# Performance work log

Measured on AMD Instinct MI355X. Metric: run time of the kernel, lower is better.

Reference implementation:

```python
import jax, jax.numpy as jnp
import numpy as np
from jax import lax

B, S, IN, D, E, NH = 8, 128, 512, 1024, 4, 16
DH = D // NH
EPS = 1e-5
SCALE = np.float32(1.0 / np.sqrt(DH))


def setup_inputs() -> dict:
    key = jax.random.key(0)
    ks = iter(jax.random.split(key, 64))
    def rn(shape, scale=0.02):
        return jax.random.normal(next(ks), shape, dtype=jnp.float32) * scale
    z = lambda shape: jnp.zeros(shape, dtype=jnp.float32)
    return {
        "x": jax.random.normal(next(ks), (B, S, IN), dtype=jnp.float32),
        "router_w": rn((IN, E)), "router_b": z((E,)),
        "enc_w1": rn((E, IN, D)), "enc_b1": z((E, D)),
        "enc_w2": rn((E, D, D)), "enc_b2": z((E, D)),
        "enc_g": jnp.ones((E, D), jnp.float32), "enc_beta": z((E, D)),
        "attn_in_w": rn((E, D, 3 * D)), "attn_in_b": z((E, 3 * D)),
        "attn_out_w": rn((E, D, D)), "attn_out_b": z((E, D)),
        "lstm_wi_f": rn((E, D, 4 * D)), "lstm_wh_f": rn((E, D, 4 * D)), "lstm_b_f": z((E, 4 * D)),
        "lstm_wi_b": rn((E, D, 4 * D)), "lstm_wh_b": rn((E, D, 4 * D)), "lstm_b_b": z((E, 4 * D)),
        "sig_w1": rn((E, 2 * D, D)), "sig_b1": z((E, D)),
        "sig_w2": rn((E, D, D)), "sig_b2": z((E, D)),
        "tan_w1": rn((E, 2 * D, D)), "tan_b1": z((E, D)),
        "tan_w2": rn((E, D, D)), "tan_b2": z((E, D)),
        "dec_w1": rn((E, D, D)), "dec_b1": z((E, D)),
        "dec_w2": rn((E, D, IN)), "dec_b2": z((E, IN)),
        "dec_g": jnp.ones((E, IN), jnp.float32), "dec_beta": z((E, IN)),
    }


def _ln(x, g, b):
    m = x.mean(-1, keepdims=True)
    v = ((x - m) ** 2).mean(-1, keepdims=True)
    return (x - m) * lax.rsqrt(v + EPS) * g + b


def _lstm_dir(x, Wi, Wh, b):
    # x: [B,S,D]; single-direction LSTM, returns h sequence [B,S,H]
    bsz = x.shape[0]
    h0 = jnp.zeros((bsz, Wh.shape[0]), x.dtype)
    def step(carry, xt):
        h, c = carry
        zg = xt @ Wi + h @ Wh + b  # [B,4H]; torch gate order i,f,g,o
        i, f, g, o = jnp.split(zg, 4, axis=-1)
        c = jax.nn.sigmoid(f) * c + jax.nn.sigmoid(i) * jnp.tanh(g)
        h = jax.nn.sigmoid(o) * jnp.tanh(c)
        return (h, c), h
    _, hs = lax.scan(step, (h0, h0), jnp.swapaxes(x, 0, 1))
    return jnp.swapaxes(hs, 0, 1)


def _expert(x, p):
    (ew1, eb1, ew2, eb2, eg, ebeta, aiw, aib, aow, aob,
     wif, whf, bf, wibk, whbk, bbk, sw1, sb1, sw2, sb2,
     tw1, tb1, tw2, tb2, dw1, db1, dw2, db2, dg, dbeta) = p
    # encoder MLP + LayerNorm
    h = _ln(jax.nn.relu(x @ ew1 + eb1) @ ew2 + eb2, eg, ebeta)  # [B,S,D]
    # full self-attention (torch MultiheadAttention)
    qkv = h @ aiw + aib
    q, k, v = jnp.split(qkv, 3, axis=-1)
    def heads(t):
        return t.reshape(t.shape[0], t.shape[1], NH, DH).transpose(0, 2, 1, 3)
    q, k, v = heads(q), heads(k), heads(v)
    attn = jax.nn.softmax(jnp.einsum('bhqd,bhkd->bhqk', q, k) * SCALE, axis=-1)
    o = jnp.einsum('bhqk,bhkd->bhqd', attn, v).transpose(0, 2, 1, 3).reshape(h.shape)
    h = o @ aow + aob
    # bidirectional LSTM memory
    hf = _lstm_dir(h, wif, whf, bf)
    hb = _lstm_dir(h[:, ::-1], wibk, whbk, bbk)[:, ::-1]
    mem = jnp.concatenate([hf, hb], axis=-1)  # [B,S,2D]
    # sigmoid/tanh gate branches multiplied
    gate_s = jax.nn.sigmoid(jax.nn.relu(mem @ sw1 + sb1) @ sw2 + sb2)
    gate_t = jnp.tanh(jax.nn.relu(mem @ tw1 + tb1) @ tw2 + tb2)
    g = gate_s * gate_t  # [B,S,D]
    # decoder MLP + LayerNorm back to input_dim
    return _ln(jax.nn.relu(g @ dw1 + db1) @ dw2 + db2, dg, dbeta)


def _forward(x, router_w, router_b, *p):
    outs = jax.vmap(lambda pe: _expert(x, pe))(tuple(p))  # [E,B,S,IN]
    w = jax.nn.softmax(x @ router_w + router_b, axis=-1)  # [B,S,E] token-level routing
    return jnp.einsum('ebsd,bse->bsd', outs, w)


def reference(x, router_w, router_b, enc_w1, enc_b1, enc_w2, enc_b2, enc_g, enc_beta,
              attn_in_w, attn_in_b, attn_out_w, attn_out_b,
              lstm_wi_f, lstm_wh_f, lstm_b_f, lstm_wi_b, lstm_wh_b, lstm_b_b,
              sig_w1, sig_b1, sig_w2, sig_b2, tan_w1, tan_b1, tan_w2, tan_b2,
              dec_w1, dec_b1, dec_w2, dec_b2, dec_g, dec_beta):
    return _forward(x, router_w, router_b, enc_w1, enc_b1, enc_w2, enc_b2, enc_g, enc_beta,
                    attn_in_w, attn_in_b, attn_out_w, attn_out_b,
                    lstm_wi_f, lstm_wh_f, lstm_b_f, lstm_wi_b, lstm_wh_b, lstm_b_b,
                    sig_w1, sig_b1, sig_w2, sig_b2, tan_w1, tan_b1, tan_w2, tan_b2,
                    dec_w1, dec_b1, dec_w2, dec_b2, dec_g, dec_beta)
```

## Files before the change

kernel.cpp:

```cpp
#include <hip/hip_runtime.h>


typedef __attribute__((ext_vector_type(8))) short short8v;
typedef __attribute__((ext_vector_type(4))) float float4v;

__device__ __forceinline__ float bf2f(unsigned short u) {
    unsigned int x = ((unsigned int)u) << 16;
    return __builtin_bit_cast(float, x);
}
__device__ __forceinline__ unsigned short f2bf(float f) {
    unsigned int u = __builtin_bit_cast(unsigned int, f);
    u += 0x7fffu + ((u >> 16) & 1u);
    return (unsigned short)(u >> 16);
}
__device__ __forceinline__ void gload_lds16(const unsigned short* g, unsigned short* lds) {
    __builtin_amdgcn_global_load_lds(
        (const __attribute__((address_space(1))) unsigned int*)g,
        (__attribute__((address_space(3))) unsigned int*)lds, 16, 0, 0);
}

__global__ __launch_bounds__(256) void cvt_bf16_kernel(
    const float* __restrict__ in, unsigned short* __restrict__ out, int n4)
{
    int i = blockIdx.x * 256 + threadIdx.x;
    if (i >= n4) return;
    float4 v = *reinterpret_cast<const float4*>(&in[i * 4]);
    ushort4 o;
    o.x = f2bf(v.x); o.y = f2bf(v.y); o.z = f2bf(v.z); o.w = f2bf(v.w);
    *reinterpret_cast<ushort4*>(&out[i * 4]) = o;
}

struct TransJobs {
    const float* src[14];
    unsigned short* dst[14];
    int K[14], N[14];
    int prefix[15];
    long sWe[14], sTe[14];
};

__global__ __launch_bounds__(256) void transpose_all(TransJobs J)
{
    __shared__ float tile[32][33];
    int bid = blockIdx.x;
    int j = 0;
    #pragma unroll
    for (int i = 0; i < 14; ++i) if (bid >= J.prefix[i + 1]) j = i + 1;
    int lb = bid - J.prefix[j];
    int K = J.K[j], N = J.N[j];
    int tn = N >> 5, tk = K >> 5;
    int e = lb / (tn * tk), rem = lb % (tn * tk);
    int ky = rem / tn, nx = rem % tn;
    const float* W = J.src[j] + (long)e * J.sWe[j];
    unsigned short* Wt = J.dst[j] + (long)e * J.sTe[j];
    int k0 = ky * 32, n0 = nx * 32;
    int tx = threadIdx.x & 31, ty = threadIdx.x >> 5;
    #pragma unroll
    for (int i = 0; i < 32; i += 8)
        tile[ty + i][tx] = W[(long)(k0 + ty + i) * N + n0 + tx];
    __syncthreads();
    #pragma unroll
    for (int i = 0; i < 32; i += 8)
        Wt[(long)(n0 + ty + i) * K + k0 + tx] = f2bf(tile[tx][ty + i]);
}

__global__ __launch_bounds__(64) void router_kernel(
    const float* __restrict__ x, const float* __restrict__ rw,
    const float* __restrict__ rb, float* __restrict__ router)
{
    int token = blockIdx.x;
    int lane = threadIdx.x;
    float a0 = 0.f, a1 = 0.f, a2 = 0.f, a3 = 0.f;
    const float* xp = x + (long)token * 512;
    for (int i = lane; i < 512; i += 64) {
        float xv = xp[i];
        const float* w = rw + (long)i * 4;
        a0 += xv * w[0]; a1 += xv * w[1]; a2 += xv * w[2]; a3 += xv * w[3];
    }
    #pragma unroll
    for (int off = 32; off; off >>= 1) {
        a0 += __shfl_down(a0, off); a1 += __shfl_down(a1, off);
        a2 += __shfl_down(a2, off); a3 += __shfl_down(a3, off);
    }
    if (lane == 0) {
        a0 += rb[0]; a1 += rb[1]; a2 += rb[2]; a3 += rb[3];
        float m = fmaxf(fmaxf(a0, a1), fmaxf(a2, a3));
        float e0 = __expf(a0 - m), e1 = __expf(a1 - m);
        float e2 = __expf(a2 - m), e3 = __expf(a3 - m);
        float inv = 1.f / (e0 + e1 + e2 + e3);
        *reinterpret_cast<float4*>(&router[token * 4]) =
            make_float4(e0 * inv, e1 * inv, e2 * inv, e3 * inv);
    }
}

template <int OUTBF>
__global__ __launch_bounds__(256) void gemm_bf16(
    const unsigned short* __restrict__ A, const unsigned short* __restrict__ Wt,
    const float* __restrict__ bias, const float* __restrict__ bias2,
    const unsigned short* __restrict__ mul,
    void* __restrict__ Cv, int N, int K, int lda, int nsplit,
    long sAe, long sWe, long sBe, long sMe, long sCe, int act)
{
    __shared__ unsigned short As[2][128 * 64];
    __shared__ unsigned short Bs[2][128 * 64];
    int e = blockIdx.z;
    A += (long)e * sAe; Wt += (long)e * sWe;
    bias += (long)e * sBe; bias2 += (long)e * sBe;
    if (mul) mul += (long)e * sMe;
    int tid = threadIdx.x;
    int row0 = blockIdx.y * 128, col0 = blockIdx.x * 128;
    int wid = tid >> 6, lane = tid & 63;
    int wr = wid >> 1, wc = wid & 1;
    int l15 = lane & 15, l4 = lane >> 4;
    int r8 = lane >> 3, sg = lane & 7;
    float4v acc[4][4];
    #pragma unroll
    for (int i = 0; i < 4; ++i)
        #pragma unroll
        for (int j = 0; j < 4; ++j) acc[i][j] = (float4v){0.f, 0.f, 0.f, 0.f};

    auto STAGE = [&](int buf, int k0) {
        #pragma unroll
        for (int c = 0; c < 4; ++c) {
            int chunk = wid * 4 + c;
            int rowA = chunk * 8 + r8;
            int segA = (sg ^ (rowA & 7)) * 8;
            gload_lds16(A + (long)(row0 + rowA) * lda + k0 + segA,
                        (unsigned short*)((char*)As[buf] + chunk * 1024));
            gload_lds16(Wt + (long)(col0 + rowA) * K + k0 + segA,
                        (unsigned short*)((char*)Bs[buf] + chunk * 1024));
        }
    };
    int nt = K >> 6;
    STAGE(0, 0);
    for (int t = 0; t < nt; ++t) {
        int cur = t & 1;
        if (t + 1 < nt) {
            STAGE(cur ^ 1, (t + 1) << 6);
            asm volatile("s_waitcnt vmcnt(8)" ::: "memory");
        } else {
            asm volatile("s_waitcnt vmcnt(0)" ::: "memory");
        }
        __builtin_amdgcn_s_barrier();
        __builtin_amdgcn_sched_barrier(0);
        #pragma unroll
        for (int kk = 0; kk < 2; ++kk) {
            short8v af[4], bq[4];
            int bytec = kk * 64 + l4 * 16;
            #pragma unroll
            for (int m = 0; m < 4; ++m) {
                int r = wr * 64 + m * 16 + l15;
                af[m] = *reinterpret_cast<const short8v*>(
                    (char*)As[cur] + r * 128 + (bytec ^ ((r & 7) << 4)));
            }
            #pragma unroll
            for (int n = 0; n < 4; ++n) {
                int r = wc * 64 + n * 16 + l15;
                bq[n] = *reinterpret_cast<const short8v*>(
                    (char*)Bs[cur] + r * 128 + (bytec ^ ((r & 7) << 4)));
            }
            #pragma unroll
            for (int m = 0; m < 4; ++m)
                #pragma unroll
                for (int n = 0; n < 4; ++n)
                    acc[m][n] = __builtin_amdgcn_mfma_f32_16x16x32_bf16(
                        af[m], bq[n], acc[m][n], 0, 0, 0);
        }
        __builtin_amdgcn_sched_barrier(0);
        __builtin_amdgcn_s_barrier();
    }
    float* Cf = (float*)Cv + (long)e * sCe;
    unsigned short* Cb = (unsigned short*)Cv + (long)e * sCe;
    #pragma unroll
    for (int n = 0; n < 4; ++n) {
        int col = col0 + wc * 64 + n * 16 + l15;
        float bia = (col < nsplit) ? bias[col] : bias2[col - nsplit];
        #pragma unroll
        for (int m = 0; m < 4; ++m) {
            #pragma unroll
            for (int r = 0; r < 4; ++r) {
                long row = row0 + wr * 64 + m * 16 + l4 * 4 + r;
                float v = acc[m][n][r] + bia;
                if (act == 1) v = fmaxf(v, 0.f);
                else if (act == 2) v = 1.f / (1.f + __expf(-v));
                else if (act == 3) v = tanhf(v);
                if (mul) v *= bf2f(mul[row * N + col]);
                if (OUTBF) Cb[row * N + col] = f2bf(v);
                else       Cf[row * N + col] = v;
            }
        }
    }
}

template <int DIM>
__global__ __launch_bounds__(256) void ln_bf16(
    unsigned short* __restrict__ buf, const float* __restrict__ g,
    const float* __restrict__ beta)
{
    constexpr int PT = DIM / 256;
    __shared__ float sbuf[4];
    int row = blockIdx.x, e = row >> 10;
    unsigned short* p = buf + (long)row * DIM;
    const float* gp = g + (long)e * DIM;
    const float* bp = beta + (long)e * DIM;
    int tid = threadIdx.x;
    float v[PT];
    ushort4 u = *reinterpret_cast<const ushort4*>(p + tid * PT);
    v[0] = bf2f(u.x); v[1] = bf2f(u.y); v[2] = bf2f(u.z); v[3] = bf2f(u.w);
    float s = v[0] + v[1] + v[2] + v[3];
    #pragma unroll
    for (int off = 32; off; off >>= 1) s += __shfl_down(s, off);
    if ((tid & 63) == 0) sbuf[tid >> 6] = s;
    __syncthreads();
    float mean = (sbuf[0] + sbuf[1] + sbuf[2] + sbuf[3]) / (float)DIM;
    __syncthreads();
    float vs = 0.f;
    #pragma unroll
    for (int i = 0; i < PT; ++i) { float d = v[i] - mean; vs += d * d; }
    #pragma unroll
    for (int off = 32; off; off >>= 1) vs += __shfl_down(vs, off);
    if ((tid & 63) == 0) sbuf[tid >> 6] = vs;
    __syncthreads();
    float var = (sbuf[0] + sbuf[1] + sbuf[2] + sbuf[3]) / (float)DIM;
    float rstd = rsqrtf(var + 1e-5f);
    ushort4 o;
    o.x = f2bf((v[0] - mean) * rstd * gp[tid * PT + 0] + bp[tid * PT + 0]);
    o.y = f2bf((v[1] - mean) * rstd * gp[tid * PT + 1] + bp[tid * PT + 1]);
    o.z = f2bf((v[2] - mean) * rstd * gp[tid * PT + 2] + bp[tid * PT + 2]);
    o.w = f2bf((v[3] - mean) * rstd * gp[tid * PT + 3] + bp[tid * PT + 3]);
    *reinterpret_cast<ushort4*>(p + tid * PT) = o;
}

template <int DIM>
__global__ __launch_bounds__(256) void ln_kernel(
    float* __restrict__ buf, const float* __restrict__ g,
    const float* __restrict__ beta)
{
    constexpr int PT = DIM / 256;
    __shared__ float sbuf[4];
    int row = blockIdx.x, e = row >> 10;
    float* p = buf + (long)row * DIM;
    const float* gp = g + (long)e * DIM;
    const float* bp = beta + (long)e * DIM;
    int tid = threadIdx.x;
    float v[PT];
    float s = 0.f;
    #pragma unroll
    for (int i = 0; i < PT; ++i) { v[i] = p[tid + i * 256]; s += v[i]; }
    #pragma unroll
    for (int off = 32; off; off >>= 1) s += __shfl_down(s, off);
    if ((tid & 63) == 0) sbuf[tid >> 6] = s;
    __syncthreads();
    float mean = (sbuf[0] + sbuf[1] + sbuf[2] + sbuf[3]) / (float)DIM;
    __syncthreads();
    float vs = 0.f;
    #pragma unroll
    for (int i = 0; i < PT; ++i) { float d = v[i] - mean; vs += d * d; }
    #pragma unroll
    for (int off = 32; off; off >>= 1) vs += __shfl_down(vs, off);
    if ((tid & 63) == 0) sbuf[tid >> 6] = vs;
    __syncthreads();
    float var = (sbuf[0] + sbuf[1] + sbuf[2] + sbuf[3]) / (float)DIM;
    float rstd = rsqrtf(var + 1e-5f);
    #pragma unroll
    for (int i = 0; i < PT; ++i)
        p[tid + i * 256] = (v[i] - mean) * rstd * gp[tid + i * 256] + bp[tid + i * 256];
}

__global__ __launch_bounds__(128) void attn_bf16(
    const unsigned short* __restrict__ qkv, unsigned short* __restrict__ o)
{
    __shared__ __align__(16) float Ks[128][64];
    __shared__ __align__(16) float Vs[128][64];
    int id = blockIdx.x;
    int hd = id & 15, b = (id >> 4) & 7, e = id >> 7;
    int tid = threadIdx.x;
    const long base = ((long)e * 1024 + b * 128) * 3072 + hd * 64;
    #pragma unroll
    for (int i = 0; i < 8; ++i) {
        int idx = i * 128 + tid;
        int row = idx >> 3, f8 = (idx & 7) * 8;
        short8v kv = *reinterpret_cast<const short8v*>(&qkv[base + (long)row * 3072 + 1024 + f8]);
        short8v vv = *reinterpret_cast<const short8v*>(&qkv[base + (long)row * 3072 + 2048 + f8]);
        #pragma unroll
        for (int j = 0; j < 8; ++j) {
            Ks[row][f8 + j] = bf2f((unsigned short)kv[j]);
            Vs[row][f8 + j] = bf2f((unsigned short)vv[j]);
        }
    }
    __syncthreads();
    float q[64];
    #pragma unroll
    for (int f = 0; f < 8; ++f) {
        short8v qv = *reinterpret_cast<const short8v*>(&qkv[base + (long)tid * 3072 + f * 8]);
        #pragma unroll
        for (int j = 0; j < 8; ++j) q[f * 8 + j] = bf2f((unsigned short)qv[j]);
    }
    float m = -__builtin_huge_valf(), l = 0.f;
    float oa[64];
    #pragma unroll
    for (int d = 0; d < 64; ++d) oa[d] = 0.f;
    for (int j = 0; j < 128; ++j) {
        float s = 0.f;
        #pragma unroll
        for (int d = 0; d < 64; ++d) s = fmaf(q[d], Ks[j][d], s);
        s *= 0.125f;
        float mn = fmaxf(m, s);
        float corr = __expf(m - mn);
        float pj = __expf(s - mn);
        l = l * corr + pj;
        #pragma unroll
        for (int d = 0; d < 64; ++d) oa[d] = oa[d] * corr + pj * Vs[j][d];
        m = mn;
    }
    float inv = 1.f / l;
    unsigned short* op = o + ((long)e * 1024 + b * 128 + tid) * 1024 + hd * 64;
    #pragma unroll
    for (int f = 0; f < 8; ++f) {
        short8v ov;
        #pragma unroll
        for (int j = 0; j < 8; ++j) ov[j] = (short)f2bf(oa[f * 8 + j] * inv);
        *reinterpret_cast<short8v*>(&op[f * 8]) = ov;
    }
}

__global__ __launch_bounds__(512, 4) void lstm_persistent(
    const unsigned short* __restrict__ pre, const unsigned short* __restrict__ whtf,
    const unsigned short* __restrict__ whtb, unsigned short* __restrict__ hstate,
    unsigned short* __restrict__ memb, unsigned int* __restrict__ sync)
{
    __shared__ unsigned short hA[16 * 1024];
    __shared__ float zred[4][2][8][16];
    int bid = blockIdx.x;
    int ed = bid & 7, cb = bid >> 3;
    int e = ed >> 1, dir = ed & 1;
    const unsigned short* Wt = (dir ? whtb : whtf) + (long)e * 4096 * 1024;
    unsigned int* arr = sync + ed * 64;
    int tid = threadIdx.x;
    int w = tid >> 6, lane = tid & 63, l15 = lane & 15, l4 = lane >> 4;
    int g = w >> 1, kh = w & 1;
    short8v wf[16];
    const unsigned short* wp =
        Wt + ((long)(g * 1024 + cb * 16 + l15)) * 1024 + kh * 512 + l4 * 8;
    #pragma unroll
    for (int ks = 0; ks < 16; ++ks)
        wf[ks] = *reinterpret_cast<const short8v*>(wp + ks * 32);
    short8v z8 = {0, 0, 0, 0, 0, 0, 0, 0};
    for (int i = tid; i < 8 * 128; i += 512) {
        int r = 8 + (i >> 7), sb = (i & 127) * 16;
        *reinterpret_cast<short8v*>((char*)hA + r * 2048 + (sb ^ ((r & 7) << 4))) = z8;
    }
    float c0 = 0.f, c1 = 0.f;
    int gp = tid & 7, gb = tid >> 3;
    for (int s = 0; s < 128; ++s) {
        int t = dir ? 127 - s : s;
        const unsigned long long* hin64 = reinterpret_cast<const unsigned long long*>(
            hstate + (long)(s & 1) * 65536 + (long)ed * 8192);
        __syncthreads();
        #pragma unroll
        for (int i = 0; i < 4; ++i) {
            int idx = tid + 512 * i;
            unsigned long long v = __hip_atomic_load(
                hin64 + idx, __ATOMIC_RELAXED, __HIP_MEMORY_SCOPE_AGENT);
            int r = idx >> 8, sb = (idx & 255) * 8;
            *reinterpret_cast<unsigned long long*>(
                (char*)hA + r * 2048 + (sb ^ ((r & 7) << 4))) = v;
        }
        float pz[8];
        if (tid < 64) {
            const unsigned short* prow =
                pre + (((long)e * 1024) + gb * 128 + t) * 8192 + dir * 4096 + cb * 16 + gp * 2;
            #pragma unroll
            for (int gg = 0; gg < 4; ++gg) {
                unsigned int u = *reinterpret_cast<const unsigned int*>(prow + gg * 1024);
                pz[gg * 2]     = bf2f((unsigned short)(u & 0xffff));
                pz[gg * 2 + 1] = bf2f((unsigned short)(u >> 16));
            }
        }
        __syncthreads();
        float4v acc = (float4v){0.f, 0.f, 0.f, 0.f};
        int abase = l15 * 2048, aswz = (l15 & 7) << 4;
        #pragma unroll
        for (int ks = 0; ks < 16; ++ks) {
            short8v a = *reinterpret_cast<const short8v*>(
                (char*)hA + abase + (((kh * 512 + ks * 32) * 2 + l4 * 16) ^ aswz));
            acc = __builtin_amdgcn_mfma_f32_16x16x32_bf16(a, wf[ks], acc, 0, 0, 0);
        }
        if (l4 < 2) {
            #pragma unroll
            for (int r = 0; r < 4; ++r)
                zred[g][kh][l4 * 4 + r][l15] = acc[r];
        }
        __syncthreads();
        if (tid < 64) {
            int col0 = gp * 2;
            float h2[2];
            #pragma unroll
            for (int cc = 0; cc < 2; ++cc) {
                int col = col0 + cc;
                float zi = zred[0][0][gb][col] + zred[0][1][gb][col] + pz[0 + cc];
                float zf = zred[1][0][gb][col] + zred[1][1][gb][col] + pz[2 + cc];
                float zg = zred[2][0][gb][col] + zred[2][1][gb][col] + pz[4 + cc];
                float zo = zred[3][0][gb][col] + zred[3][1][gb][col] + pz[6 + cc];
                float ig = 1.f / (1.f + __expf(-zi));
                float fg = 1.f / (1.f + __expf(-zf));
                float gv = tanhf(zg);
                float og = 1.f / (1.f + __expf(-zo));
                float cv = cc ? c1 : c0;
                cv = fg * cv + ig * gv;
                if (cc) c1 = cv; else c0 = cv;
                h2[cc] = og * tanhf(cv);
            }
            unsigned int hv = (unsigned int)f2bf(h2[0]) | ((unsigned int)f2bf(h2[1]) << 16);
            int hcol = cb * 16 + col0;
            unsigned int* hout32 = reinterpret_cast<unsigned int*>(
                hstate + (long)((s & 1) ^ 1) * 65536 + (long)ed * 8192);
            __hip_atomic_store(hout32 + (gb * 1024 + hcol) / 2, hv,
                               __ATOMIC_RELAXED, __HIP_MEMORY_SCOPE_AGENT);
            *reinterpret_cast<unsigned int*>(
                memb + (((long)e * 8 + gb) * 128 + t) * 2048 + dir * 1024 + hcol) = hv;
        }
        if (s == 127) break;
        __syncthreads();
        if (tid == 0)
            __hip_atomic_store(arr + cb, (unsigned)(s + 1), __ATOMIC_RELAXED,
                               __HIP_MEMORY_SCOPE_AGENT);
        if (tid < 64) {
            while (__hip_atomic_load(arr + tid, __ATOMIC_RELAXED,
                                     __HIP_MEMORY_SCOPE_AGENT) < (unsigned)(s + 1))
                __builtin_amdgcn_s_sleep(1);
        }
    }
}

__global__ __launch_bounds__(256) void combine_kernel(
    const float* __restrict__ outs, const float* __restrict__ router,
    float* __restrict__ out)
{
    int idx = blockIdx.x * 256 + threadIdx.x;
    int token = idx >> 7, q = (idx & 127) * 4;
    float4 r = *reinterpret_cast<const float4*>(&router[token * 4]);
    const float* bp = outs + (long)token * 512 + q;
    float4 v0 = *reinterpret_cast<const float4*>(bp);
    float4 v1 = *reinterpret_cast<const float4*>(bp + 524288);
    float4 v2 = *reinterpret_cast<const float4*>(bp + 1048576);
    float4 v3 = *reinterpret_cast<const float4*>(bp + 1572864);
    float4 a;
    a.x = r.x * v0.x + r.y * v1.x + r.z * v2.x + r.w * v3.x;
    a.y = r.x * v0.y + r.y * v1.y + r.z * v2.y + r.w * v3.y;
    a.z = r.x * v0.z + r.y * v1.z + r.z * v2.z + r.w * v3.z;
    a.w = r.x * v0.w + r.y * v1.w + r.z * v2.w + r.w * v3.w;
    *reinterpret_cast<float4*>(&out[(long)token * 512 + q]) = a;
}

extern "C" void kernel_launch(void* const* d_in, const int* in_sizes, int n_in,
                              void* d_out, int out_size, void* d_ws, size_t ws_size,
                              hipStream_t stream)
{
    (void)in_sizes; (void)n_in; (void)out_size; (void)ws_size;
    const float* x        = (const float*)d_in[0];
    const float* router_w = (const float*)d_in[1];
    const float* router_b = (const float*)d_in[2];
    const float* enc_w1   = (const float*)d_in[3];
    const float* enc_b1   = (const float*)d_in[4];
    const float* enc_w2   = (const float*)d_in[5];
    const float* enc_b2   = (const float*)d_in[6];
    const float* enc_g    = (const float*)d_in[7];
    const float* enc_beta = (const float*)d_in[8];
    const float* aiw      = (const float*)d_in[9];
    const float* aib      = (const float*)d_in[10];
    const float* aow      = (const float*)d_in[11];
    const float* aob      = (const float*)d_in[12];
    const float* wif      = (const float*)d_in[13];
    const float* whf      = (const float*)d_in[14];
    const float* bfv      = (const float*)d_in[15];
    const float* wib      = (const float*)d_in[16];
    const float* whb      = (const float*)d_in[17];
    const float* bbv      = (const float*)d_in[18];
    const float* sw1      = (const float*)d_in[19];
    const float* sb1      = (const float*)d_in[20];
    const float* sw2      = (const float*)d_in[21];
    const float* sb2      = (const float*)d_in[22];
    const float* tw1      = (const float*)d_in[23];
    const float* tb1      = (const float*)d_in[24];
    const float* tw2      = (const float*)d_in[25];
    const float* tb2      = (const float*)d_in[26];
    const float* dw1      = (const float*)d_in[27];
    const float* db1      = (const float*)d_in[28];
    const float* dw2      = (const float*)d_in[29];
    const float* db2      = (const float*)d_in[30];
    const float* dg       = (const float*)d_in[31];
    const float* dbeta    = (const float*)d_in[32];
    float* out = (float*)d_out;

    const long m = 1024L * 1024L;
    unsigned short* U = (unsigned short*)d_ws;
    unsigned short* ew1T = U;
    unsigned short* ew2T = U + 2 * m;
    unsigned short* aiwT = U + 6 * m;
    unsigned short* aowT = U + 18 * m;
    unsigned short* wiT  = U + 22 * m;
    unsigned short* whtf = U + 54 * m;
    unsigned short* whtb = U + 70 * m;
    unsigned short* gw1T = U + 86 * m;
    unsigned short* sw2T = U + 102 * m;
    unsigned short* tw2T = U + 106 * m;
    unsigned short* dw1T = U + 110 * m;
    unsigned short* dw2T = U + 114 * m;
    unsigned short* xb   = U + 116 * m;
    unsigned short* hbuf = xb + 524288;
    unsigned short* t1   = hbuf + 4 * m;
    unsigned short* t2   = t1 + 4 * m;
    unsigned short* pre  = t2 + 4 * m;
    unsigned short* memb = pre + 32 * m;
    unsigned short* hstate = memb + 8 * m;
    float* F      = (float*)(U + 170 * m);
    float* outs   = F;
    float* router = outs + 2 * m;
    unsigned int* syncv = (unsigned int*)(router + 4096);

    hipMemsetAsync(hstate, 0, 65536 * sizeof(unsigned short), stream);
    hipMemsetAsync(syncv, 0, 1024 * sizeof(unsigned int), stream);

    cvt_bf16_kernel<<<512, 256, 0, stream>>>(x, xb, 131072);
    {
        TransJobs J;
        const float* srcs[14] = {enc_w1, enc_w2, aiw, aow, wif, wib, whf, whb,
                                 sw1, tw1, sw2, tw2, dw1, dw2};
        unsigned short* dsts[14] = {ew1T, ew2T, aiwT, aowT, wiT, wiT + 4096 * 1024L,
                                    whtf, whtb, gw1T, gw1T + 2 * m, sw2T, tw2T, dw1T, dw2T};
        int Ks[14] = {512, 1024, 1024, 1024, 1024, 1024, 1024, 1024,
                      2048, 2048, 1024, 1024, 1024, 1024};
        int Ns[14] = {1024, 1024, 3072, 1024, 4096, 4096, 4096, 4096,
                      1024, 1024, 1024, 1024, 1024, 512};
        long sWes[14] = {512 * 1024L, m, 3 * m, m, 4 * m, 4 * m, 4 * m, 4 * m,
                         2 * m, 2 * m, m, m, m, 512 * 1024L};
        long sTes[14] = {512 * 1024L, m, 3 * m, m, 8 * m, 8 * m, 4 * m, 4 * m,
                         4 * m, 4 * m, m, m, m, 512 * 1024L};
        int pfx = 0;
        J.prefix[0] = 0;
        for (int i = 0; i < 14; ++i) {
            J.src[i] = srcs[i]; J.dst[i] = dsts[i];
            J.K[i] = Ks[i]; J.N[i] = Ns[i];
            J.sWe[i] = sWes[i]; J.sTe[i] = sTes[i];
            pfx += (Ns[i] >> 5) * (Ks[i] >> 5) * 4;
            J.prefix[i + 1] = pfx;
        }
        transpose_all<<<pfx, 256, 0, stream>>>(J);
    }

    router_kernel<<<1024, 64, 0, stream>>>(x, router_w, router_b, router);

    gemm_bf16<1><<<dim3(8, 8, 4), 256, 0, stream>>>(xb, ew1T, enc_b1, enc_b1, nullptr, t1,
        1024, 512, 512, 1024, 0L, 512 * 1024L, 1024L, 0L, m, 1);
    gemm_bf16<1><<<dim3(8, 8, 4), 256, 0, stream>>>(t1, ew2T, enc_b2, enc_b2, nullptr, hbuf,
        1024, 1024, 1024, 1024, m, m, 1024L, 0L, m, 0);
    ln_bf16<1024><<<4096, 256, 0, stream>>>(hbuf, enc_g, enc_beta);
    gemm_bf16<1><<<dim3(24, 8, 4), 256, 0, stream>>>(hbuf, aiwT, aib, aib, nullptr, pre,
        3072, 1024, 1024, 3072, m, 3 * m, 3072L, 0L, 3 * m, 0);
    attn_bf16<<<512, 128, 0, stream>>>(pre, t1);
    gemm_bf16<1><<<dim3(8, 8, 4), 256, 0, stream>>>(t1, aowT, aob, aob, nullptr, hbuf,
        1024, 1024, 1024, 1024, m, m, 1024L, 0L, m, 0);
    gemm_bf16<1><<<dim3(64, 8, 4), 256, 0, stream>>>(hbuf, wiT, bfv, bbv, nullptr, pre,
        8192, 1024, 1024, 4096, m, 8 * m, 4096L, 0L, 8 * m, 0);
    lstm_persistent<<<512, 512, 0, stream>>>(pre, whtf, whtb, hstate, memb, syncv);
    unsigned short* g1o = pre;
    gemm_bf16<1><<<dim3(16, 8, 4), 256, 0, stream>>>(memb, gw1T, sb1, tb1, nullptr, g1o,
        2048, 2048, 2048, 1024, 2 * m, 4 * m, 1024L, 0L, 2 * m, 1);
    gemm_bf16<1><<<dim3(8, 8, 4), 256, 0, stream>>>(g1o, sw2T, sb2, sb2, nullptr, t2,
        1024, 1024, 2048, 1024, 2 * m, m, 1024L, 0L, m, 2);
    gemm_bf16<1><<<dim3(8, 8, 4), 256, 0, stream>>>(g1o + 1024, tw2T, tb2, tb2, t2, hbuf,
        1024, 1024, 2048, 1024, 2 * m, m, 1024L, m, m, 3);
    gemm_bf16<1><<<dim3(8, 8, 4), 256, 0, stream>>>(hbuf, dw1T, db1, db1, nullptr, t1,
        1024, 1024, 1024, 1024, m, m, 1024L, 0L, m, 1);
    gemm_bf16<0><<<dim3(4, 8, 4), 256, 0, stream>>>(t1, dw2T, db2, db2, nullptr, outs,
        512, 1024, 1024, 512, m, 512 * 1024L, 512L, 0L, 512 * 1024L, 0);
    ln_kernel<512><<<4096, 256, 0, stream>>>(outs, dg, dbeta);
    combine_kernel<<<512, 256, 0, stream>>>(outs, router, out);
}
```

Baseline: 1.306 ms.

## Replace LSTM inter-block barrier with tagged-data flags embedded in hidden state

The persistent LSTM kernel no longer uses a separate per-step arrival counter and spin barrier. Each block now writes the hidden state as fp32, with the low mantissa bit carrying a parity tag that encodes the step. Consumers poll the state words directly until every tag matches, then convert to bf16 in LDS. This removes one __syncthreads, the counter store and the barrier round trip on the serial 128-step critical path, at the cost of twice the hidden-state traffic, more polling loads per thread, and a small precision change from overwriting the mantissa bit.

Result: slower. 1.769 ms (+35.4%).

```diff
diff --git a/kernel.cpp b/kernel.cpp
--- a/kernel.cpp
+++ b/kernel.cpp
@@ -325,8 +325,8 @@
 
 __global__ __launch_bounds__(512, 4) void lstm_persistent(
     const unsigned short* __restrict__ pre, const unsigned short* __restrict__ whtf,
-    const unsigned short* __restrict__ whtb, unsigned short* __restrict__ hstate,
-    unsigned short* __restrict__ memb, unsigned int* __restrict__ sync)
+    const unsigned short* __restrict__ whtb, float* __restrict__ hstate,
+    unsigned short* __restrict__ memb)
 {
     __shared__ unsigned short hA[16 * 1024];
     __shared__ float zred[4][2][8][16];
@@ -334,7 +334,6 @@
     int ed = bid & 7, cb = bid >> 3;
     int e = ed >> 1, dir = ed & 1;
     const unsigned short* Wt = (dir ? whtb : whtf) + (long)e * 4096 * 1024;
-    unsigned int* arr = sync + ed * 64;
     int tid = threadIdx.x;
     int w = tid >> 6, lane = tid & 63, l15 = lane & 15, l4 = lane >> 4;
     int g = w >> 1, kh = w & 1;
@@ -353,18 +352,10 @@
     int gp = tid & 7, gb = tid >> 3;
     for (int s = 0; s < 128; ++s) {
         int t = dir ? 127 - s : s;
+        unsigned tag_r = (s == 0) ? 0u : ((((unsigned)(s - 1)) >> 1) + 1u) & 1u;
         const unsigned long long* hin64 = reinterpret_cast<const unsigned long long*>(
             hstate + (long)(s & 1) * 65536 + (long)ed * 8192);
         __syncthreads();
-        #pragma unroll
-        for (int i = 0; i < 4; ++i) {
-            int idx = tid + 512 * i;
-            unsigned long long v = __hip_atomic_load(
-                hin64 + idx, __ATOMIC_RELAXED, __HIP_MEMORY_SCOPE_AGENT);
-            int r = idx >> 8, sb = (idx & 255) * 8;
-            *reinterpret_cast<unsigned long long*>(
-                (char*)hA + r * 2048 + (sb ^ ((r & 7) << 4))) = v;
-        }
         float pz[8];
         if (tid < 64) {
             const unsigned short* prow =
@@ -375,6 +366,40 @@
                 pz[gg * 2]     = bf2f((unsigned short)(u & 0xffff));
                 pz[gg * 2 + 1] = bf2f((unsigned short)(u >> 16));
             }
+        }
+        unsigned long long v[8];
+        #pragma unroll
+        for (int i = 0; i < 8; ++i)
+            v[i] = __hip_atomic_load(hin64 + tid + 512 * i,
+                                     __ATOMIC_RELAXED, __HIP_MEMORY_SCOPE_AGENT);
+        unsigned pend = 0xffu;
+        while (true) {
+            unsigned np = 0;
+            #pragma unroll
+            for (int i = 0; i < 8; ++i) {
+                if (pend & (1u << i)) {
+                    unsigned lo = (unsigned)v[i], hi = (unsigned)(v[i] >> 32);
+                    if ((((lo ^ tag_r) | (hi ^ tag_r)) & 1u)) np |= 1u << i;
+                }
+            }
+            if (!np) break;
+            __builtin_amdgcn_s_sleep(1);
+            #pragma unroll
+            for (int i = 0; i < 8; ++i)
+                if (np & (1u << i))
+                    v[i] = __hip_atomic_load(hin64 + tid + 512 * i,
+                                             __ATOMIC_RELAXED, __HIP_MEMORY_SCOPE_AGENT);
+            pend = np;
+        }
+        #pragma unroll
+        for (int i = 0; i < 8; ++i) {
+            int idx = tid + 512 * i;
+            float f0 = __builtin_bit_cast(float, (unsigned)v[i]);
+            float f1 = __builtin_bit_cast(float, (unsigned)(v[i] >> 32));
+            unsigned hv = (unsigned)f2bf(f0) | ((unsigned)f2bf(f1) << 16);
+            int r = idx >> 9, ob = (idx & 511) * 4;
+            *reinterpret_cast<unsigned*>(
+                (char*)hA + r * 2048 + (ob ^ ((r & 7) << 4))) = hv;
         }
         __syncthreads();
         float4v acc = (float4v){0.f, 0.f, 0.f, 0.f};
@@ -410,24 +435,19 @@
                 if (cc) c1 = cv; else c0 = cv;
                 h2[cc] = og * tanhf(cv);
             }
-            unsigned int hv = (unsigned int)f2bf(h2[0]) | ((unsigned int)f2bf(h2[1]) << 16);
             int hcol = cb * 16 + col0;
-            unsigned int* hout32 = reinterpret_cast<unsigned int*>(
+            unsigned hv = (unsigned)f2bf(h2[0]) | ((unsigned)f2bf(h2[1]) << 16);
+            *reinterpret_cast<unsigned*>(
+                memb + (((long)e * 8 + gb) * 128 + t) * 2048 + dir * 1024 + hcol) = hv;
+            unsigned tw = ((((unsigned)s) >> 1) + 1u) & 1u;
+            unsigned u0 = (__builtin_bit_cast(unsigned, h2[0]) & ~1u) | tw;
+            unsigned u1 = (__builtin_bit_cast(unsigned, h2[1]) & ~1u) | tw;
+            unsigned long long uv = (unsigned long long)u0 |
+                                    ((unsigned long long)u1 << 32);
+            unsigned long long* hout64 = reinterpret_cast<unsigned long long*>(
                 hstate + (long)((s & 1) ^ 1) * 65536 + (long)ed * 8192);
-            __hip_atomic_store(hout32 + (gb * 1024 + hcol) / 2, hv,
+            __hip_atomic_store(hout64 + (gb * 1024 + hcol) / 2, uv,
                                __ATOMIC_RELAXED, __HIP_MEMORY_SCOPE_AGENT);
-            *reinterpret_cast<unsigned int*>(
-                memb + (((long)e * 8 + gb) * 128 + t) * 2048 + dir * 1024 + hcol) = hv;
-        }
-        if (s == 127) break;
-        __syncthreads();
-        if (tid == 0)
-            __hip_atomic_store(arr + cb, (unsigned)(s + 1), __ATOMIC_RELAXED,
-                               __HIP_MEMORY_SCOPE_AGENT);
-        if (tid < 64) {
-            while (__hip_atomic_load(arr + tid, __ATOMIC_RELAXED,
-                                     __HIP_MEMORY_SCOPE_AGENT) < (unsigned)(s + 1))
-                __builtin_amdgcn_s_sleep(1);
         }
     }
 }
@@ -512,14 +532,12 @@
     unsigned short* t2   = t1 + 4 * m;
     unsigned short* pre  = t2 + 4 * m;
     unsigned short* memb = pre + 32 * m;
-    unsigned short* hstate = memb + 8 * m;
     float* F      = (float*)(U + 170 * m);
     float* outs   = F;
     float* router = outs + 2 * m;
-    unsigned int* syncv = (unsigned int*)(router + 4096);
-
-    hipMemsetAsync(hstate, 0, 65536 * sizeof(unsigned short), stream);
-    hipMemsetAsync(syncv, 0, 1024 * sizeof(unsigned int), stream);
+    float* hstateF = router + 4096;
+
+    hipMemsetAsync(hstateF, 0, 65536 * sizeof(float), stream);
 
     cvt_bf16_kernel<<<512, 256, 0, stream>>>(x, xb, 131072);
     {
@@ -562,7 +580,7 @@
         1024, 1024, 1024, 1024, m, m, 1024L, 0L, m, 0);
     gemm_bf16<1><<<dim3(64, 8, 4), 256, 0, stream>>>(hbuf, wiT, bfv, bbv, nullptr, pre,
         8192, 1024, 1024, 4096, m, 8 * m, 4096L, 0L, 8 * m, 0);
-    lstm_persistent<<<512, 512, 0, stream>>>(pre, whtf, whtb, hstate, memb, syncv);
+    lstm_persistent<<<512, 512, 0, stream>>>(pre, whtf, whtb, hstateF, memb);
     unsigned short* g1o = pre;
     gemm_bf16<1><<<dim3(16, 8, 4), 256, 0, stream>>>(memb, gw1T, sb1, tb1, nullptr, g1o,
         2048, 2048, 2048, 1024, 2 * m, 4 * m, 1024L, 0L, 2 * m, 1);
```

## Replace LSTM per-step counter barrier with sentinel-poisoned h sequence polling

Applied to the files above, without the earlier changes.

The persistent LSTM kernel no longer uses a per-step atomic counter barrier across blocks. Each step's hidden state goes to its own slot in a sequence buffer pre-filled with a 0x7f7f sentinel, and readers spin on the data itself until no sentinel values remain. This removes one barrier round-trip and the extra __syncthreads per timestep. It also swaps tanhf for an exp-based fast tanh. The risks are that a real bf16 value equal to 0x7f7f would cause a hang, and that the fast tanh loses some accuracy and can produce NaN for large inputs where exp overflows.

After: 1.419 ms. 1.09x slower.

```diff
diff --git a/kernel.cpp b/kernel.cpp
--- a/kernel.cpp
+++ b/kernel.cpp
@@ -17,6 +17,15 @@
     __builtin_amdgcn_global_load_lds(
         (const __attribute__((address_space(1))) unsigned int*)g,
         (__attribute__((address_space(3))) unsigned int*)lds, 16, 0, 0);
+}
+__device__ __forceinline__ float ftanh(float x) {
+    float e = __expf(2.f * x);
+    return 1.f - 2.f / (e + 1.f);
+}
+__device__ __forceinline__ bool stale8(unsigned long long x) {
+    unsigned lo = (unsigned)x, hi = (unsigned)(x >> 32);
+    return ((lo & 0xffffu) == 0x7f7fu) | ((lo >> 16) == 0x7f7fu) |
+           ((hi & 0xffffu) == 0x7f7fu) | ((hi >> 16) == 0x7f7fu);
 }
 
 __global__ __launch_bounds__(256) void cvt_bf16_kernel(
@@ -182,7 +191,7 @@
                 float v = acc[m][n][r] + bia;
                 if (act == 1) v = fmaxf(v, 0.f);
                 else if (act == 2) v = 1.f / (1.f + __expf(-v));
-                else if (act == 3) v = tanhf(v);
+                else if (act == 3) v = ftanh(v);
                 if (mul) v *= bf2f(mul[row * N + col]);
                 if (OUTBF) Cb[row * N + col] = f2bf(v);
                 else       Cf[row * N + col] = v;
@@ -325,8 +334,8 @@
 
 __global__ __launch_bounds__(512, 4) void lstm_persistent(
     const unsigned short* __restrict__ pre, const unsigned short* __restrict__ whtf,
-    const unsigned short* __restrict__ whtb, unsigned short* __restrict__ hstate,
-    unsigned short* __restrict__ memb, unsigned int* __restrict__ sync)
+    const unsigned short* __restrict__ whtb, unsigned short* __restrict__ hseq,
+    unsigned short* __restrict__ memb)
 {
     __shared__ unsigned short hA[16 * 1024];
     __shared__ float zred[4][2][8][16];
@@ -334,7 +343,6 @@
     int ed = bid & 7, cb = bid >> 3;
     int e = ed >> 1, dir = ed & 1;
     const unsigned short* Wt = (dir ? whtb : whtf) + (long)e * 4096 * 1024;
-    unsigned int* arr = sync + ed * 64;
     int tid = threadIdx.x;
     int w = tid >> 6, lane = tid & 63, l15 = lane & 15, l4 = lane >> 4;
     int g = w >> 1, kh = w & 1;
@@ -354,17 +362,8 @@
     for (int s = 0; s < 128; ++s) {
         int t = dir ? 127 - s : s;
         const unsigned long long* hin64 = reinterpret_cast<const unsigned long long*>(
-            hstate + (long)(s & 1) * 65536 + (long)ed * 8192);
+            hseq + ((long)s * 8 + ed) * 8192);
         __syncthreads();
-        #pragma unroll
-        for (int i = 0; i < 4; ++i) {
-            int idx = tid + 512 * i;
-            unsigned long long v = __hip_atomic_load(
-                hin64 + idx, __ATOMIC_RELAXED, __HIP_MEMORY_SCOPE_AGENT);
-            int r = idx >> 8, sb = (idx & 255) * 8;
-            *reinterpret_cast<unsigned long long*>(
-                (char*)hA + r * 2048 + (sb ^ ((r & 7) << 4))) = v;
-        }
         float pz[8];
         if (tid < 64) {
             const unsigned short* prow =
@@ -375,6 +374,34 @@
                 pz[gg * 2]     = bf2f((unsigned short)(u & 0xffff));
                 pz[gg * 2 + 1] = bf2f((unsigned short)(u >> 16));
             }
+        }
+        unsigned long long v[4];
+        #pragma unroll
+        for (int i = 0; i < 4; ++i)
+            v[i] = __hip_atomic_load(hin64 + tid + 512 * i,
+                                     __ATOMIC_RELAXED, __HIP_MEMORY_SCOPE_AGENT);
+        unsigned pend = 0xfu;
+        while (true) {
+            unsigned np = 0;
+            #pragma unroll
+            for (int i = 0; i < 4; ++i)
+                if ((pend >> i) & 1u)
+                    if (stale8(v[i])) np |= 1u << i;
+            if (!np) break;
+            __builtin_amdgcn_s_sleep(1);
+            #pragma unroll
+            for (int i = 0; i < 4; ++i)
+                if ((np >> i) & 1u)
+                    v[i] = __hip_atomic_load(hin64 + tid + 512 * i,
+                                             __ATOMIC_RELAXED, __HIP_MEMORY_SCOPE_AGENT);
+            pend = np;
+        }
+        #pragma unroll
+        for (int i = 0; i < 4; ++i) {
+            int idx = tid + 512 * i;
+            int r = idx >> 8, sb = (idx & 255) * 8;
+            *reinterpret_cast<unsigned long long*>(
+                (char*)hA + r * 2048 + (sb ^ ((r & 7) << 4))) = v[i];
         }
         __syncthreads();
         float4v acc = (float4v){0.f, 0.f, 0.f, 0.f};
@@ -403,31 +430,21 @@
                 float zo = zred[3][0][gb][col] + zred[3][1][gb][col] + pz[6 + cc];
                 float ig = 1.f / (1.f + __expf(-zi));
                 float fg = 1.f / (1.f + __expf(-zf));
-                float gv = tanhf(zg);
+                float gv = ftanh(zg);
                 float og = 1.f / (1.f + __expf(-zo));
                 float cv = cc ? c1 : c0;
                 cv = fg * cv + ig * gv;
                 if (cc) c1 = cv; else c0 = cv;
-                h2[cc] = og * tanhf(cv);
+                h2[cc] = og * ftanh(cv);
             }
             unsigned int hv = (unsigned int)f2bf(h2[0]) | ((unsigned int)f2bf(h2[1]) << 16);
             int hcol = cb * 16 + col0;
             unsigned int* hout32 = reinterpret_cast<unsigned int*>(
-                hstate + (long)((s & 1) ^ 1) * 65536 + (long)ed * 8192);
+                hseq + ((long)(s + 1) * 8 + ed) * 8192);
             __hip_atomic_store(hout32 + (gb * 1024 + hcol) / 2, hv,
                                __ATOMIC_RELAXED, __HIP_MEMORY_SCOPE_AGENT);
             *reinterpret_cast<unsigned int*>(
                 memb + (((long)e * 8 + gb) * 128 + t) * 2048 + dir * 1024 + hcol) = hv;
-        }
-        if (s == 127) break;
-        __syncthreads();
-        if (tid == 0)
-            __hip_atomic_store(arr + cb, (unsigned)(s + 1), __ATOMIC_RELAXED,
-                               __HIP_MEMORY_SCOPE_AGENT);
-        if (tid < 64) {
-            while (__hip_atomic_load(arr + tid, __ATOMIC_RELAXED,
-                                     __HIP_MEMORY_SCOPE_AGENT) < (unsigned)(s + 1))
-                __builtin_amdgcn_s_sleep(1);
         }
     }
 }
@@ -512,14 +529,10 @@
     unsigned short* t2   = t1 + 4 * m;
     unsigned short* pre  = t2 + 4 * m;
     unsigned short* memb = pre + 32 * m;
-    unsigned short* hstate = memb + 8 * m;
     float* F      = (float*)(U + 170 * m);
     float* outs   = F;
     float* router = outs + 2 * m;
-    unsigned int* syncv = (unsigned int*)(router + 4096);
-
-    hipMemsetAsync(hstate, 0, 65536 * sizeof(unsigned short), stream);
-    hipMemsetAsync(syncv, 0, 1024 * sizeof(unsigned int), stream);
+    unsigned short* hseq = U;
 
     cvt_bf16_kernel<<<512, 256, 0, stream>>>(x, xb, 131072);
     {
@@ -562,7 +575,10 @@
         1024, 1024, 1024, 1024, m, m, 1024L, 0L, m, 0);
     gemm_bf16<1><<<dim3(64, 8, 4), 256, 0, stream>>>(hbuf, wiT, bfv, bbv, nullptr, pre,
         8192, 1024, 1024, 4096, m, 8 * m, 4096L, 0L, 8 * m, 0);
-    lstm_persistent<<<512, 512, 0, stream>>>(pre, whtf, whtb, hstate, memb, syncv);
+    hipMemsetAsync(hseq, 0, 8 * 8192 * sizeof(unsigned short), stream);
+    hipMemsetAsync(hseq + 8 * 8192, 0x7f,
+                   128L * 8 * 8192 * sizeof(unsigned short), stream);
+    lstm_persistent<<<512, 512, 0, stream>>>(pre, whtf, whtb, hseq, memb);
     unsigned short* g1o = pre;
     gemm_bf16<1><<<dim3(16, 8, 4), 256, 0, stream>>>(memb, gw1T, sb1, tb1, nullptr, g1o,
         2048, 2048, 2048, 1024, 2 * m, 4 * m, 1024L, 0L, 2 * m, 1);
```
